# Performance work log

Hardware: AMD Instinct MI355X
Metric: run time of the kernel (lower is better)

## Reference

```python
import jax, jax.numpy as jnp
import numpy as np

N = 32768       # batch of states
DQ = 8          # q_ndim (dof_ndim)
A = 4           # action_dim
H = 1024        # hidden_size


def setup_inputs() -> dict:
    key = jax.random.key(0)
    ks = jax.random.split(key, 16)

    def lin(kw, kb, fan_out, fan_in, zero_bias=False):
        s = 1.0 / np.sqrt(fan_in)
        W = jax.random.normal(kw, (fan_out, fan_in), dtype=jnp.float32) * s
        b = jnp.zeros((fan_out,), jnp.float32) if zero_bias else \
            jax.random.normal(kb, (fan_out,), dtype=jnp.float32) * s
        return W, b

    W1, b1 = lin(ks[0], ks[1], H, 2 * DQ)            # h_net layer 1
    W2, b2 = lin(ks[2], ks[3], H, H)                 # h_net layer 2
    Wh, bh = lin(ks[4], ks[5], 1, H)                 # h_net head -> scalar H(z)
    Wf1, bf1 = lin(ks[6], ks[7], H, 2 * DQ + A)      # flex_net layer 1
    Wf2, bf2 = lin(ks[8], ks[9], H, H)               # flex_net layer 2
    Wff, bff = lin(ks[10], ks[11], 2 * DQ, H)        # flex_net head -> 2*q_ndim
    Wp, bp = lin(ks[12], ks[13], A, 2 * DQ)          # control policy (detached)

    return {
        "t": jnp.zeros((), jnp.float32),
        "z": jax.random.normal(ks[14], (N, 2 * DQ), dtype=jnp.float32),
        "W1": W1, "b1": b1, "W2": W2, "b2": b2, "Wh": Wh, "bh": bh,
        "Wf1": Wf1, "bf1": bf1, "Wf2": Wf2, "bf2": bf2, "Wff": Wff, "bff": bff,
        "Wp": Wp, "bp": bp,
    }


def reference(t, z, W1, b1, W2, b2, Wh, bh,
              Wf1, bf1, Wf2, bf2, Wff, bff, Wp, bp):
    # control input, detached as in the torch forward (u = policy(t, z).detach())
    u = jax.lax.stop_gradient(jnp.tanh(z @ Wp.T + bp))  # [N, A]

    # ---- H-net forward, saving tanh' at each activation (the `sps` list) ----
    # angular_dims=() -> CosSin is the identity, so h_net[0](z) = z.
    a1 = z @ W1.T + b1          # [N, H]
    h1 = jnp.tanh(a1)
    s0 = 1.0 - h1 * h1          # d tanh / d a1   (sps[0])
    a2 = h1 @ W2.T + b2         # [N, H]
    h2 = jnp.tanh(a2)
    s1 = 1.0 - h2 * h2          # d tanh / d a2   (sps[1])

    # dH = grad_z sum(h_net(z)), with gradients flowing (create_graph=True)
    def H_sum(zz):
        hh = jnp.tanh(zz @ W1.T + b1)
        hh = jnp.tanh(hh @ W2.T + b2)
        return jnp.sum(hh @ Wh.T + bh)

    dH = jax.grad(H_sum)(z)     # [N, 2*DQ]

    # ---- flex-net with skip term modulated by reversed tanh' maps ----
    zu = jnp.concatenate([z, u], axis=-1)       # [N, 2*DQ + A]
    f1 = zu @ Wf1.T + bf1
    g1 = jnp.tanh(f1) + f1 * s1                 # idx = 1 -> sps[1]
    f2 = g1 @ Wf2.T + bf2
    g2 = jnp.tanh(f2) + f2 * s0                 # idx = 0 -> sps[0]
    out = g2 @ Wff.T + bff                      # [N, 2*DQ]

    # D = jacobian of CosSin = identity per batch row (angular_dims=()), so
    # bmm(out[:,None,:], D).squeeze(1) == out.

    # dz_dt = J @ (out + dH):  J([top; bot]) = [bot; -top]
    s = out + dH
    return jnp.concatenate([s[:, DQ:], -s[:, :DQ]], axis=-1)  # [N, 2*DQ]
```

## Files before the change

kernel.cpp:

```cpp
#include <hip/hip_runtime.h>
#include <hip/hip_bf16.h>

typedef __hip_bfloat16 bf16;
typedef __attribute__((ext_vector_type(8))) short short8;
typedef __attribute__((ext_vector_type(4))) short s16x4;
typedef __attribute__((ext_vector_type(4))) float f32x4;

__device__ __forceinline__ bf16 f2b(float f) { return __float2bfloat16(f); }
__device__ __forceinline__ short bfbits(float f) {
  union { float f; unsigned u; } x; x.f = f;
  unsigned r = x.u + 0x7fff + ((x.u >> 16) & 1);
  return (short)(r >> 16);
}
__device__ __forceinline__ float tanh_fast(float x) {
  float t = __expf(-2.f * fabsf(x));
  float r = (1.f - t) * __builtin_amdgcn_rcpf(1.f + t);
  return copysignf(r, x);
}

#define GLOAD_LDS16(gp, lp) __builtin_amdgcn_global_load_lds( \
    (const __attribute__((address_space(1))) void*)(gp), \
    (__attribute__((address_space(3))) void*)(lp), 16, 0, 0)

__global__ __launch_bounds__(256) void prep(
    const float* __restrict__ W2, const float* __restrict__ Wf2,
    const float* __restrict__ W1, const float* __restrict__ Wff,
    bf16* __restrict__ W2bf, bf16* __restrict__ W2Tbf,
    bf16* __restrict__ Wf2bf, bf16* __restrict__ W1n,
    bf16* __restrict__ Wffn)
{
  __shared__ float T[32][33];
  const int tid = threadIdx.x, bx = blockIdx.x;
  const int tx = bx & 31, ty = bx >> 5;
  const int r = tid >> 3, c4 = (tid & 7) * 4;
  const long ibase = (long)(ty * 32 + r) * 1024 + tx * 32 + c4;

  f32x4 v = *(const f32x4*)(W2 + ibase);
  f32x4 vf = *(const f32x4*)(Wf2 + ibase);
  s16x4 sv, sf;
  #pragma unroll
  for (int j = 0; j < 4; ++j) {
    sv[j] = bfbits(v[j]); sf[j] = bfbits(vf[j]);
    T[r][c4 + j] = v[j];
  }
  *(s16x4*)(W2bf + ibase) = sv;
  *(s16x4*)(Wf2bf + ibase) = sf;
  __syncthreads();
  const int oc = tid >> 3, or4 = (tid & 7) * 4;
  s16x4 st;
  #pragma unroll
  for (int j = 0; j < 4; ++j) st[j] = bfbits(T[or4 + j][oc]);
  *(s16x4*)(W2Tbf + (long)(tx * 32 + oc) * 1024 + ty * 32 + or4) = st;

  if (bx < 32) {
    #pragma unroll
    for (int rep = 0; rep < 2; ++rep) {
      int i = bx * 512 + rep * 256 + tid;
      int rr = i >> 10, cc = i & 1023;
      W1n[i] = f2b(W1[cc * 16 + rr]);
      Wffn[i] = f2b(Wff[i]);
    }
  }
}

__global__ __launch_bounds__(256) void k1(
    const float* __restrict__ z, const float* __restrict__ W1,
    const float* __restrict__ b1, const float* __restrict__ Wp,
    const float* __restrict__ bp, const float* __restrict__ Wf1,
    const float* __restrict__ bf1v,
    bf16* __restrict__ h1, bf16* __restrict__ f1out, long grow0)
{
  __shared__ float zs[32][16];
  __shared__ float us[32][4];
  const int tid = threadIdx.x;
  const long r0 = (long)blockIdx.x * 32;
  for (int i = tid; i < 512; i += 256) {
    int r = i >> 4, c = i & 15;
    zs[r][c] = z[(grow0 + r0 + r) * 16 + c];
  }
  __syncthreads();
  if (tid < 128) {
    int r = tid >> 2, a = tid & 3;
    float acc = bp[a];
    #pragma unroll
    for (int k = 0; k < 16; ++k) acc = fmaf(zs[r][k], Wp[a * 16 + k], acc);
    us[r][a] = tanh_fast(acc);
  }
  __syncthreads();
  #pragma unroll
  for (int jj = 0; jj < 4; ++jj) {
    const int c = tid + jj * 256;
    {
      float w[16];
      #pragma unroll
      for (int k = 0; k < 16; ++k) w[k] = W1[c * 16 + k];
      const float bc = b1[c];
      for (int r = 0; r < 32; ++r) {
        float a = bc;
        #pragma unroll
        for (int k = 0; k < 16; ++k) a = fmaf(zs[r][k], w[k], a);
        h1[(r0 + r) * 1024 + c] = f2b(tanh_fast(a));
      }
    }
    {
      float wf[20];
      #pragma unroll
      for (int k = 0; k < 20; ++k) wf[k] = Wf1[c * 20 + k];
      const float bfc = bf1v[c];
      for (int r = 0; r < 32; ++r) {
        float f = bfc;
        #pragma unroll
        for (int k = 0; k < 16; ++k) f = fmaf(zs[r][k], wf[k], f);
        #pragma unroll
        for (int a = 0; a < 4; ++a) f = fmaf(us[r][a], wf[16 + a], f);
        f1out[(r0 + r) * 1024 + c] = f2b(f);
      }
    }
  }
}

template<int EPI>
__global__ __launch_bounds__(512, 2) void gemm_k(
    const bf16* __restrict__ A, const bf16* __restrict__ Bp,
    const float* __restrict__ bias, const float* __restrict__ Whv,
    const bf16* __restrict__ h1,
    bf16* O1, bf16* __restrict__ O2,
    const bf16* __restrict__ Wn, float* __restrict__ Pp, int ckRows)
{
  constexpr int SMEM = (EPI == 0) ? 65536 : 69632;
  __shared__ __align__(16) char smem[SMEM];
  const int tid = threadIdx.x;
  const int lane = tid & 63, wid = tid >> 6;
  const int wr = wid >> 2, wc = wid & 3;
  const int fr = lane & 15, kg = lane >> 4;
  const long row0 = (long)blockIdx.x * 256;
  const int col0 = blockIdx.y * 256;

  const int sr0 = tid >> 2;
  const int sk0 = ((tid & 3) ^ ((tid >> 3) & 3)) * 8;
  const int swr = (fr >> 1) & 3;

  const bf16* gA0 = A + (row0 + sr0) * 1024 + sk0;
  const bf16* gB0 = Bp + ((long)col0 + sr0) * 1024 + sk0;
  const int rdA = (wr * 128 + fr) * 32 + (kg ^ swr) * 8;
  const int rdB = (wc * 64 + fr) * 32 + (kg ^ swr) * 8;

  f32x4 acc[8][4] = {};

  {
    bf16* as = (bf16*)smem;
    bf16* bs = (bf16*)smem + 16384;
    GLOAD_LDS16(gA0, as + tid * 8);
    GLOAD_LDS16(gA0 + 128 * 1024, as + 4096 + tid * 8);
    GLOAD_LDS16(gB0, bs + tid * 8);
    GLOAD_LDS16(gB0 + 128 * 1024, bs + 4096 + tid * 8);
  }
  __syncthreads();

  #pragma unroll 2
  for (int kt = 0; kt < 32; ++kt) {
    const int cur = kt & 1;
    if (kt < 31) {
      const int k0 = (kt + 1) * 32;
      bf16* as = (bf16*)smem + (cur ^ 1) * 8192;
      bf16* bs = (bf16*)smem + 16384 + (cur ^ 1) * 8192;
      GLOAD_LDS16(gA0 + k0, as + tid * 8);
      GLOAD_LDS16(gA0 + 128 * 1024 + k0, as + 4096 + tid * 8);
      GLOAD_LDS16(gB0 + k0, bs + tid * 8);
      GLOAD_LDS16(gB0 + 128 * 1024 + k0, bs + 4096 + tid * 8);
    }
    const bf16* as = (const bf16*)smem + cur * 8192;
    const bf16* bs = (const bf16*)smem + 16384 + cur * 8192;
    short8 af[8], bfr[4];
    #pragma unroll
    for (int m = 0; m < 8; ++m)
      af[m] = *(const short8*)(as + rdA + m * 512);
    #pragma unroll
    for (int n = 0; n < 4; ++n)
      bfr[n] = *(const short8*)(bs + rdB + n * 512);
    #pragma unroll
    for (int m = 0; m < 8; ++m)
      #pragma unroll
      for (int n = 0; n < 4; ++n)
        acc[m][n] = __builtin_amdgcn_mfma_f32_16x16x32_bf16(af[m], bfr[n], acc[m][n], 0, 0, 0);
    __syncthreads();
  }

  if (EPI == 0) {
    #pragma unroll
    for (int m = 0; m < 8; ++m) {
      const long gr0 = row0 + wr * 128 + m * 16 + kg * 4;
      #pragma unroll
      for (int n = 0; n < 4; ++n) {
        const int gc = col0 + wc * 64 + n * 16 + fr;
        const float b2c = bias[gc], whc = Whv[gc];
        f32x4 v = acc[m][n];
        #pragma unroll
        for (int j = 0; j < 4; ++j) {
          const long idx = (gr0 + j) * 1024 + gc;
          float h = tanh_fast(v[j] + b2c);
          float s1v = 1.f - h * h;
          float f = __bfloat162float(((const bf16*)O1)[idx]);
          O2[idx] = f2b(s1v * whc);
          O1[idx] = f2b(tanh_fast(f) + f * s1v);
        }
      }
    }
  } else {
    bf16* Ot = (bf16*)smem;
    f32x4 pacc[2] = {};
    #pragma unroll
    for (int ph = 0; ph < 2; ++ph) {
      if ((wc >> 1) == ph) {
        #pragma unroll
        for (int m = 0; m < 8; ++m) {
          const int rl0 = wr * 128 + m * 16 + kg * 4;
          const long gr0 = row0 + rl0;
          #pragma unroll
          for (int n = 0; n < 4; ++n) {
            const int cl = (wc & 1) * 64 + n * 16 + fr;
            const int gc = col0 + ph * 128 + cl;
            f32x4 v = acc[m][n];
            #pragma unroll
            for (int j = 0; j < 4; ++j) {
              const long idx = (gr0 + j) * 1024 + gc;
              float x = v[j], g;
              if (EPI == 1) {
                float hh = __bfloat162float(h1[idx]);
                g = x * (1.f - hh * hh);
              } else {
                float f = x + bias[gc];
                float hh = __bfloat162float(h1[idx]);
                g = tanh_fast(f) + f * (1.f - hh * hh);
              }
              Ot[(rl0 + j) * 136 + cl] = f2b(g);
            }
          }
        }
      }
      __syncthreads();
      #pragma unroll
      for (int sub = 0; sub < 2; ++sub) {
        const int rl0 = wid * 32 + sub * 16;
        #pragma unroll
        for (int ks = 0; ks < 4; ++ks) {
          short8 afrag = *(const short8*)(Ot + (rl0 + fr) * 136 + ks * 32 + kg * 8);
          short8 bfrag = *(const short8*)(Wn + fr * 1024 + col0 + ph * 128 + ks * 32 + kg * 8);
          pacc[sub] = __builtin_amdgcn_mfma_f32_16x16x32_bf16(afrag, bfrag, pacc[sub], 0, 0, 0);
        }
      }
      if (ph == 0) __syncthreads();
    }
    #pragma unroll
    for (int sub = 0; sub < 2; ++sub) {
      const int rl0 = wid * 32 + sub * 16;
      #pragma unroll
      for (int j = 0; j < 4; ++j)
        Pp[(((long)blockIdx.y) * ckRows + row0 + rl0 + kg * 4 + j) * 16 + fr] = pacc[sub][j];
    }
  }
}

__global__ __launch_bounds__(256) void k7(
    const float* __restrict__ Pp0, const float* __restrict__ Pp1,
    const float* __restrict__ bff, float* __restrict__ out,
    long grow0, int ckRows)
{
  int i = blockIdx.x * 256 + threadIdx.x;
  int r = i >> 4, j = i & 15, jp = (j + 8) & 15;
  float s = bff[jp];
  #pragma unroll
  for (int cb = 0; cb < 4; ++cb) {
    long o = ((long)cb * ckRows + r) * 16 + jp;
    s += Pp0[o] + Pp1[o];
  }
  out[(grow0 + r) * 16 + j] = (j < 8) ? s : -s;
}

extern "C" void kernel_launch(void* const* d_in, const int* in_sizes, int n_in,
                              void* d_out, int out_size, void* d_ws, size_t ws_size,
                              hipStream_t stream) {
  const float* z   = (const float*)d_in[1];
  const float* W1  = (const float*)d_in[2];
  const float* b1  = (const float*)d_in[3];
  const float* W2  = (const float*)d_in[4];
  const float* b2  = (const float*)d_in[5];
  const float* Wh  = (const float*)d_in[6];
  const float* Wf1 = (const float*)d_in[8];
  const float* bf1 = (const float*)d_in[9];
  const float* Wf2 = (const float*)d_in[10];
  const float* bf2 = (const float*)d_in[11];
  const float* Wff = (const float*)d_in[12];
  const float* bff = (const float*)d_in[13];
  const float* Wp  = (const float*)d_in[14];
  const float* bp  = (const float*)d_in[15];
  float* out = (float*)d_out;
  const int N = in_sizes[1] / 16;

  char* p = (char*)d_ws;
  auto alloc = [&](size_t bytes) {
    char* q = p; p += (bytes + 255) & ~(size_t)255; return q;
  };
  bf16* W2bf  = (bf16*)alloc(1024 * 1024 * 2);
  bf16* W2Tbf = (bf16*)alloc(1024 * 1024 * 2);
  bf16* Wf2bf = (bf16*)alloc(1024 * 1024 * 2);
  bf16* W1n   = (bf16*)alloc(16 * 1024 * 2);
  bf16* Wffn  = (bf16*)alloc(16 * 1024 * 2);
  size_t wbytes = (size_t)(p - (char*)d_ws);

  int CK = N;
  while (CK > 256 && wbytes + (size_t)CK * 6656 > ws_size) CK >>= 1;
  bf16* actA = (bf16*)alloc((size_t)CK * 2048);
  bf16* actB = (bf16*)alloc((size_t)CK * 2048);
  bf16* actD = (bf16*)alloc((size_t)CK * 2048);
  float* Pp0 = (float*)alloc((size_t)CK * 4 * 16 * 4);
  float* Pp1 = (float*)alloc((size_t)CK * 4 * 16 * 4);

  prep<<<1024, 256, 0, stream>>>(W2, Wf2, W1, Wff, W2bf, W2Tbf, Wf2bf, W1n, Wffn);

  const dim3 ggrid(CK / 256, 4);
  for (long r0 = 0; r0 < N; r0 += CK) {
    k1<<<CK / 32, 256, 0, stream>>>(z, W1, b1, Wp, bp, Wf1, bf1, actA, actD, r0);
    gemm_k<0><<<ggrid, 512, 0, stream>>>(
        actA, W2bf, b2, Wh, nullptr, actD, actB, nullptr, nullptr, CK);
    gemm_k<1><<<ggrid, 512, 0, stream>>>(
        actB, W2Tbf, nullptr, nullptr, actA, nullptr, nullptr, W1n, Pp0, CK);
    gemm_k<2><<<ggrid, 512, 0, stream>>>(
        actD, Wf2bf, bf2, nullptr, actA, nullptr, nullptr, Wffn, Pp1, CK);
    k7<<<CK / 16, 256, 0, stream>>>(Pp0, Pp1, bff, out, r0, CK);
  }
}
```

Measured before the change: 357.5 us.

## Deepen GEMM K-loop to 4-stage LDS pipeline with explicit vmcnt waits

Replaces the double-buffered K loop with a 4-buffer ring that prefetches three tiles ahead, using explicit s_waitcnt vmcnt counts and raw s_barrier instead of __syncthreads. It also raises wave priority around the MFMA block and fully unrolls the loop. The aim is to hide more global-to-LDS load latency behind compute. In exchange, LDS per block doubles to 128 KB, which likely prevents two blocks per CU and reduces occupancy.

```diff
diff --git a/kernel.cpp b/kernel.cpp
--- a/kernel.cpp
+++ b/kernel.cpp
@@ -21,6 +21,9 @@
 #define GLOAD_LDS16(gp, lp) __builtin_amdgcn_global_load_lds( \
     (const __attribute__((address_space(1))) void*)(gp), \
     (__attribute__((address_space(3))) void*)(lp), 16, 0, 0)
+#define SBAR() __builtin_amdgcn_s_barrier()
+#define WAITV(n) do { asm volatile("s_waitcnt vmcnt(" #n ")" ::: "memory"); \
+                      __builtin_amdgcn_sched_barrier(0); } while (0)
 
 __global__ __launch_bounds__(256) void prep(
     const float* __restrict__ W2, const float* __restrict__ Wf2,
@@ -127,8 +130,7 @@
     bf16* O1, bf16* __restrict__ O2,
     const bf16* __restrict__ Wn, float* __restrict__ Pp, int ckRows)
 {
-  constexpr int SMEM = (EPI == 0) ? 65536 : 69632;
-  __shared__ __align__(16) char smem[SMEM];
+  __shared__ __align__(16) char smem[131072];
   const int tid = threadIdx.x;
   const int lane = tid & 63, wid = tid >> 6;
   const int wr = wid >> 2, wc = wid & 3;
@@ -147,30 +149,23 @@
 
   f32x4 acc[8][4] = {};
 
-  {
-    bf16* as = (bf16*)smem;
-    bf16* bs = (bf16*)smem + 16384;
-    GLOAD_LDS16(gA0, as + tid * 8);
-    GLOAD_LDS16(gA0 + 128 * 1024, as + 4096 + tid * 8);
-    GLOAD_LDS16(gB0, bs + tid * 8);
-    GLOAD_LDS16(gB0 + 128 * 1024, bs + 4096 + tid * 8);
-  }
-  __syncthreads();
-
-  #pragma unroll 2
+  auto stage = [&](int b, int k0) {
+    bf16* as = (bf16*)smem + b * 8192;
+    bf16* bs = (bf16*)smem + 32768 + b * 8192;
+    GLOAD_LDS16(gA0 + k0, as + tid * 8);
+    GLOAD_LDS16(gA0 + 128 * 1024 + k0, as + 4096 + tid * 8);
+    GLOAD_LDS16(gB0 + k0, bs + tid * 8);
+    GLOAD_LDS16(gB0 + 128 * 1024 + k0, bs + 4096 + tid * 8);
+  };
+
+  stage(0, 0); stage(1, 32); stage(2, 64);
+  WAITV(8); SBAR();
+
+  #pragma unroll
   for (int kt = 0; kt < 32; ++kt) {
-    const int cur = kt & 1;
-    if (kt < 31) {
-      const int k0 = (kt + 1) * 32;
-      bf16* as = (bf16*)smem + (cur ^ 1) * 8192;
-      bf16* bs = (bf16*)smem + 16384 + (cur ^ 1) * 8192;
-      GLOAD_LDS16(gA0 + k0, as + tid * 8);
-      GLOAD_LDS16(gA0 + 128 * 1024 + k0, as + 4096 + tid * 8);
-      GLOAD_LDS16(gB0 + k0, bs + tid * 8);
-      GLOAD_LDS16(gB0 + 128 * 1024 + k0, bs + 4096 + tid * 8);
-    }
-    const bf16* as = (const bf16*)smem + cur * 8192;
-    const bf16* bs = (const bf16*)smem + 16384 + cur * 8192;
+    if (kt + 3 < 32) stage((kt + 3) & 3, (kt + 3) * 32);
+    const bf16* as = (const bf16*)smem + (kt & 3) * 8192;
+    const bf16* bs = (const bf16*)smem + 32768 + (kt & 3) * 8192;
     short8 af[8], bfr[4];
     #pragma unroll
     for (int m = 0; m < 8; ++m)
@@ -178,12 +173,17 @@
     #pragma unroll
     for (int n = 0; n < 4; ++n)
       bfr[n] = *(const short8*)(bs + rdB + n * 512);
+    __builtin_amdgcn_s_setprio(1);
     #pragma unroll
     for (int m = 0; m < 8; ++m)
       #pragma unroll
       for (int n = 0; n < 4; ++n)
         acc[m][n] = __builtin_amdgcn_mfma_f32_16x16x32_bf16(af[m], bfr[n], acc[m][n], 0, 0, 0);
-    __syncthreads();
+    __builtin_amdgcn_s_setprio(0);
+    if (kt < 29)       WAITV(8);
+    else if (kt == 29) WAITV(4);
+    else if (kt == 30) WAITV(0);
+    if (kt < 31) SBAR();
   }
 
   if (EPI == 0) {
@@ -207,6 +207,7 @@
       }
     }
   } else {
+    __syncthreads();
     bf16* Ot = (bf16*)smem;
     f32x4 pacc[2] = {};
     #pragma unroll
```

Measured after the change: 346.1 us. 1.03x faster.
